# Kernel optimization log

Measured on AMD Instinct MI355X. Metric: run time of the kernel, lower is better.

## Reference

```python
import jax, jax.numpy as jnp
import numpy as np

B, T = 32, 2048
STATE, ACT, LAT, ENC = 128, 16, 256, 1024  # input_dim = STATE + 2*ACT = 160


def setup_inputs() -> dict:
    key = jax.random.key(0)
    ks = jax.random.split(key, 16)
    s = lambda k, shp, sc=0.05: jax.random.normal(k, shp, dtype=jnp.float32) * sc
    return {
        "padded_input": jax.random.normal(ks[0], (B, T, STATE + 2 * ACT), dtype=jnp.float32),
        "enc_w1": s(ks[1], (STATE, ENC)), "enc_b1": s(ks[2], (ENC,)),
        "enc_w2": s(ks[3], (ENC, ENC)),   "enc_b2": s(ks[4], (ENC,)),
        "enc_w3": s(ks[5], (ENC, LAT)),   "enc_b3": s(ks[6], (LAT,)),
        "a_diag": jax.random.uniform(ks[7], (LAT,), minval=-0.8, maxval=0.8, dtype=jnp.float32),
        "B_w": s(ks[8], (ACT, LAT)),
        "dec_w1": s(ks[9], (LAT, ENC)),  "dec_b1": s(ks[10], (ENC,)),
        "dec_w2": s(ks[11], (ENC, ENC)), "dec_b2": s(ks[12], (ENC,)),
        "dec_w3": s(ks[13], (ENC, STATE)), "dec_b3": s(ks[14], (STATE,)),
        "nwarmup": 4,
    }


def reference(padded_input, enc_w1, enc_b1, enc_w2, enc_b2, enc_w3, enc_b3,
              a_diag, B_w, dec_w1, dec_b1, dec_w2, dec_b2, dec_w3, dec_b3,
              nwarmup):
    # slice state / actuator channels
    x_t = padded_input[:, :, :STATE]                      # [B,T,STATE]
    u_t1 = padded_input[:, :, STATE + ACT:]               # [B,T,ACT]

    def encoder(x):
        h = jnp.tanh(x @ enc_w1 + enc_b1)
        h = jnp.tanh(h @ enc_w2 + enc_b2)
        return jnp.tanh(h @ enc_w3 + enc_b3)

    def decoder(z):
        h = jnp.tanh(z @ dec_w1 + dec_b1)
        h = jnp.tanh(h @ dec_w2 + dec_b2)
        return h @ dec_w3 + dec_b3

    z_t = encoder(x_t)                                    # [B,T,LAT]
    a = jnp.clip(a_diag, -0.95, 0.95)                     # clamped diagonal of A
    Bu = u_t1 @ B_w                                       # [B,T,LAT]

    # diagonal linear recurrence with warmup resets (reset_probability=0)
    zT = jnp.swapaxes(z_t, 0, 1)                          # [T,B,LAT]
    BuT = jnp.swapaxes(Bu, 0, 1)                          # [T,B,LAT]
    ts = jnp.arange(T)

    def step(prev, inputs):
        z, bu, t = inputs
        inp = jnp.where(t <= nwarmup, z, prev)
        out = a * inp + bu
        return out, out

    _, outs = jax.lax.scan(step, z_t[:, 0, :], (zT, BuT, ts))
    z_t1 = jnp.swapaxes(outs, 0, 1)                       # [B,T,LAT]
    return decoder(z_t1)                                  # [B,T,STATE]
```

## Files before the change

### kernel.cpp

```cpp
#include <hip/hip_runtime.h>
#include <stdint.h>
#include <type_traits>

#define B_ 32
#define T_ 2048
#define STATE_ 128
#define ACT_ 16
#define LAT_ 256
#define ENC_ 1024
#define ROWS_ (B_ * T_)
#define TENC_ 128
#define MENC_ (B_ * TENC_)
#define NCHUNK_ 64
#define LCHUNK_ 32
#define SLAB_ 32768

using bf16x8 = __attribute__((ext_vector_type(8))) short;
using f32x4  = __attribute__((ext_vector_type(4))) float;
using f32x16 = __attribute__((ext_vector_type(16))) float;

__device__ __forceinline__ uint16_t f2bf(float f) {
  uint32_t u = __float_as_uint(f);
  u += 0x7fff + ((u >> 16) & 1);
  return (uint16_t)(u >> 16);
}

__device__ __forceinline__ float fast_tanh(float x) {
  float e = __expf(2.f * x);
  return 1.f - 2.f / (e + 1.f);
}

__device__ __forceinline__ void xcd_remap(int gx, int gy, int& bm, int& bn) {
  if (((gy & 7) == 0) && ((gx & (gx - 1)) == 0)) {
    const int lin  = blockIdx.y * gx + blockIdx.x;
    const int xcd  = lin & 7;
    const int slot = lin >> 3;
    const int lgx  = 31 - __clz(gx);
    bn = slot & (gx - 1);
    bm = ((slot >> lgx) << 3) + xcd;
  } else {
    bm = blockIdx.y;
    bn = blockIdx.x;
  }
}

template <bool TANH, typename OUT_T>
__device__ __forceinline__ void store4(OUT_T* C, size_t m, int N, int nb,
                                       const float* bias, f32x4 a) {
  const float4 bv = *(const float4*)(bias + nb);
  float v0 = a[0] + bv.x, v1 = a[1] + bv.y, v2 = a[2] + bv.z, v3 = a[3] + bv.w;
  if (TANH) {
    v0 = fast_tanh(v0); v1 = fast_tanh(v1);
    v2 = fast_tanh(v2); v3 = fast_tanh(v3);
  }
  if constexpr (std::is_same<OUT_T, uint16_t>::value) {
    uint32_t p0 = (uint32_t)f2bf(v0) | ((uint32_t)f2bf(v1) << 16);
    uint32_t p1 = (uint32_t)f2bf(v2) | ((uint32_t)f2bf(v3) << 16);
    uint2 p = {p0, p1};
    *(uint2*)(C + m * N + nb) = p;
  } else {
    float4 p = {v0, v1, v2, v3};
    *(float4*)(C + m * N + nb) = p;
  }
}

template <bool TANH, typename OUT_T>
__global__ __launch_bounds__(256) void gemm_bt(
    const uint16_t* __restrict__ A, const uint16_t* __restrict__ Bt,
    const float* __restrict__ bias, OUT_T* __restrict__ C,
    int M, int N, int K) {
  __shared__ uint16_t smA[128 * 64];
  __shared__ uint16_t smB[128 * 64];
  const int tid  = threadIdx.x;
  const int lane = tid & 63;
  const int wave = tid >> 6;
  const int wm = wave >> 1, wn = wave & 1;
  const int l32 = lane & 31, h = lane >> 5;

  int bm, bn;
  xcd_remap(gridDim.x, gridDim.y, bm, bn);
  const int m0 = bm * 128;
  const int n0 = bn * 128;

  const int srow = wave * 32 + (lane >> 3);
  const int sblk = lane & 7;

  f32x16 acc[2][2];
#pragma unroll
  for (int i = 0; i < 2; ++i)
#pragma unroll
    for (int j = 0; j < 2; ++j)
#pragma unroll
      for (int r = 0; r < 16; ++r) acc[i][j][r] = 0.f;

  for (int k0 = 0; k0 < K; k0 += 64) {
#pragma unroll
    for (int i = 0; i < 4; ++i) {
      const int r  = srow + i * 8;
      const int kb = sblk ^ (r & 7);
      const uint16_t* ga = A  + (size_t)(m0 + r) * K + (k0 + kb * 8);
      const uint16_t* gb = Bt + (size_t)(n0 + r) * K + (k0 + kb * 8);
      uint16_t* la = smA + (size_t)(wave * 32 + i * 8) * 64;
      uint16_t* lb = smB + (size_t)(wave * 32 + i * 8) * 64;
      __builtin_amdgcn_global_load_lds(
          (const __attribute__((address_space(1))) void*)ga,
          (__attribute__((address_space(3))) void*)la, 16, 0, 0);
      __builtin_amdgcn_global_load_lds(
          (const __attribute__((address_space(1))) void*)gb,
          (__attribute__((address_space(3))) void*)lb, 16, 0, 0);
    }
    __syncthreads();

#pragma unroll
    for (int ks = 0; ks < 4; ++ks) {
      bf16x8 af[2], bfr[2];
      const int kslot = ks * 2 + h;
#pragma unroll
      for (int mt = 0; mt < 2; ++mt) {
        const int row  = wm * 64 + mt * 32 + l32;
        const int slot = kslot ^ (row & 7);
        af[mt] = *(const bf16x8*)(smA + (size_t)row * 64 + slot * 8);
      }
#pragma unroll
      for (int nt = 0; nt < 2; ++nt) {
        const int row  = wn * 64 + nt * 32 + l32;
        const int slot = kslot ^ (row & 7);
        bfr[nt] = *(const bf16x8*)(smB + (size_t)row * 64 + slot * 8);
      }
#pragma unroll
      for (int mt = 0; mt < 2; ++mt)
#pragma unroll
        for (int nt = 0; nt < 2; ++nt)
          acc[mt][nt] = __builtin_amdgcn_mfma_f32_32x32x16_bf16(
              bfr[nt], af[mt], acc[mt][nt], 0, 0, 0);
    }
    __syncthreads();
  }

#pragma unroll
  for (int mt = 0; mt < 2; ++mt) {
    const size_t m = m0 + wm * 64 + mt * 32 + l32;
#pragma unroll
    for (int nt = 0; nt < 2; ++nt) {
#pragma unroll
      for (int q = 0; q < 4; ++q) {
        const int nb = n0 + wn * 64 + nt * 32 + q * 8 + h * 4;
        f32x4 v = {acc[mt][nt][4 * q + 0], acc[mt][nt][4 * q + 1],
                   acc[mt][nt][4 * q + 2], acc[mt][nt][4 * q + 3]};
        store4<TANH>(C, m, N, nb, bias, v);
      }
    }
  }
}

template <bool TANH, typename OUT_T>
__global__ __launch_bounds__(256, 2) void gemm_wide(
    const uint16_t* __restrict__ A, const uint16_t* __restrict__ Bt,
    const float* __restrict__ bias, OUT_T* __restrict__ C,
    int M, int N, int K) {
  __shared__ uint16_t smA[128 * 64];
  __shared__ uint16_t smB[256 * 64];
  const int tid  = threadIdx.x;
  const int lane = tid & 63;
  const int wave = tid >> 6;
  const int wm = wave >> 1, wn = wave & 1;
  const int l32 = lane & 31, h = lane >> 5;

  int bm, bn;
  xcd_remap(gridDim.x, gridDim.y, bm, bn);
  const int m0 = bm * 128;
  const int n0 = bn * 256;

  const int sr8  = lane >> 3;
  const int sblk = lane & 7;

  f32x16 acc[2][4];
#pragma unroll
  for (int i = 0; i < 2; ++i)
#pragma unroll
    for (int j = 0; j < 4; ++j)
#pragma unroll
      for (int r = 0; r < 16; ++r) acc[i][j][r] = 0.f;

  for (int k0 = 0; k0 < K; k0 += 64) {
#pragma unroll
    for (int i = 0; i < 4; ++i) {
      const int r  = wave * 32 + sr8 + i * 8;
      const int kb = sblk ^ (r & 7);
      const uint16_t* ga = A + (size_t)(m0 + r) * K + (k0 + kb * 8);
      uint16_t* la = smA + (size_t)r * 64;
      __builtin_amdgcn_global_load_lds(
          (const __attribute__((address_space(1))) void*)ga,
          (__attribute__((address_space(3))) void*)la, 16, 0, 0);
    }
#pragma unroll
    for (int i = 0; i < 8; ++i) {
      const int r  = wave * 64 + sr8 + i * 8;
      const int kb = sblk ^ (r & 7);
      const uint16_t* gb = Bt + (size_t)(n0 + r) * K + (k0 + kb * 8);
      uint16_t* lb = smB + (size_t)r * 64;
      __builtin_amdgcn_global_load_lds(
          (const __attribute__((address_space(1))) void*)gb,
          (__attribute__((address_space(3))) void*)lb, 16, 0, 0);
    }
    __syncthreads();

#pragma unroll
    for (int ks = 0; ks < 4; ++ks) {
      bf16x8 af[2], bfr[4];
      const int kslot = ks * 2 + h;
#pragma unroll
      for (int mt = 0; mt < 2; ++mt) {
        const int row  = wm * 64 + mt * 32 + l32;
        const int slot = kslot ^ (row & 7);
        af[mt] = *(const bf16x8*)(smA + (size_t)row * 64 + slot * 8);
      }
#pragma unroll
      for (int nt = 0; nt < 4; ++nt) {
        const int row  = wn * 128 + nt * 32 + l32;
        const int slot = kslot ^ (row & 7);
        bfr[nt] = *(const bf16x8*)(smB + (size_t)row * 64 + slot * 8);
      }
#pragma unroll
      for (int mt = 0; mt < 2; ++mt)
#pragma unroll
        for (int nt = 0; nt < 4; ++nt)
          acc[mt][nt] = __builtin_amdgcn_mfma_f32_32x32x16_bf16(
              bfr[nt], af[mt], acc[mt][nt], 0, 0, 0);
    }
    __syncthreads();
  }

#pragma unroll
  for (int mt = 0; mt < 2; ++mt) {
    const size_t m = m0 + wm * 64 + mt * 32 + l32;
#pragma unroll
    for (int nt = 0; nt < 4; ++nt) {
#pragma unroll
      for (int q = 0; q < 4; ++q) {
        const int nb = n0 + wn * 128 + nt * 32 + q * 8 + h * 4;
        f32x4 v = {acc[mt][nt][4 * q + 0], acc[mt][nt][4 * q + 1],
                   acc[mt][nt][4 * q + 2], acc[mt][nt][4 * q + 3]};
        store4<TANH>(C, m, N, nb, bias, v);
      }
    }
  }
}

template <bool TANH, typename OUT_T>
__global__ __launch_bounds__(256) void gemm64(
    const uint16_t* __restrict__ A, const uint16_t* __restrict__ Bt,
    const float* __restrict__ bias, OUT_T* __restrict__ C,
    int M, int N, int K) {
  __shared__ uint16_t smA[64 * 64];
  __shared__ uint16_t smB[128 * 64];
  const int tid  = threadIdx.x;
  const int lane = tid & 63;
  const int wave = tid >> 6;
  const int wm = wave >> 1, wn = wave & 1;
  const int lr = lane & 15, quad = lane >> 4;

  int bm, bn;
  xcd_remap(gridDim.x, gridDim.y, bm, bn);
  const int m0 = bm * 64;
  const int n0 = bn * 128;

  const int sr8  = lane >> 3;
  const int sblk = lane & 7;

  f32x4 vzero = {0.f, 0.f, 0.f, 0.f};
  f32x4 acc[2][4];
#pragma unroll
  for (int i = 0; i < 2; ++i)
#pragma unroll
    for (int j = 0; j < 4; ++j) acc[i][j] = vzero;

  for (int k0 = 0; k0 < K; k0 += 64) {
#pragma unroll
    for (int i = 0; i < 2; ++i) {
      const int r  = wave * 16 + sr8 + i * 8;
      const int kb = sblk ^ (r & 7);
      const uint16_t* ga = A + (size_t)(m0 + r) * K + (k0 + kb * 8);
      uint16_t* la = smA + (size_t)r * 64;
      __builtin_amdgcn_global_load_lds(
          (const __attribute__((address_space(1))) void*)ga,
          (__attribute__((address_space(3))) void*)la, 16, 0, 0);
    }
#pragma unroll
    for (int i = 0; i < 4; ++i) {
      const int r  = wave * 32 + sr8 + i * 8;
      const int kb = sblk ^ (r & 7);
      const uint16_t* gb = Bt + (size_t)(n0 + r) * K + (k0 + kb * 8);
      uint16_t* lb = smB + (size_t)r * 64;
      __builtin_amdgcn_global_load_lds(
          (const __attribute__((address_space(1))) void*)gb,
          (__attribute__((address_space(3))) void*)lb, 16, 0, 0);
    }
    __syncthreads();

#pragma unroll
    for (int ks = 0; ks < 2; ++ks) {
      bf16x8 af[2], bfr[4];
      const int slotx = (ks * 4 + quad);
#pragma unroll
      for (int mt = 0; mt < 2; ++mt) {
        const int row  = wm * 32 + mt * 16 + lr;
        const int slot = slotx ^ (lr & 7);
        af[mt] = *(const bf16x8*)(smA + (size_t)row * 64 + slot * 8);
      }
#pragma unroll
      for (int nt = 0; nt < 4; ++nt) {
        const int row  = wn * 64 + nt * 16 + lr;
        const int slot = slotx ^ (lr & 7);
        bfr[nt] = *(const bf16x8*)(smB + (size_t)row * 64 + slot * 8);
      }
#pragma unroll
      for (int mt = 0; mt < 2; ++mt)
#pragma unroll
        for (int nt = 0; nt < 4; ++nt)
          acc[mt][nt] = __builtin_amdgcn_mfma_f32_16x16x32_bf16(
              bfr[nt], af[mt], acc[mt][nt], 0, 0, 0);
    }
    __syncthreads();
  }

#pragma unroll
  for (int mt = 0; mt < 2; ++mt) {
    const size_t m = m0 + wm * 32 + mt * 16 + lr;
#pragma unroll
    for (int nt = 0; nt < 4; ++nt) {
      const int nb = n0 + wn * 64 + nt * 16 + quad * 4;
      store4<TANH>(C, m, N, nb, bias, acc[mt][nt]);
    }
  }
}

struct TArgs {
  const float* s[6];
  uint16_t* d[6];
  int R[6];
  int C[6];
};

__global__ __launch_bounds__(256) void transpose_cast(TArgs a) {
  __shared__ float tile[32][33];
  const int z = blockIdx.z;
  const float* s = a.s[z];
  uint16_t* d = a.d[z];
  const int R = a.R[z], C = a.C[z];
  const int bc = blockIdx.x * 32, br = blockIdx.y * 32;
  if (bc >= C || br >= R) return;
  const int tx = threadIdx.x & 31, ty = threadIdx.x >> 5;
#pragma unroll
  for (int i = 0; i < 32; i += 8)
    tile[ty + i][tx] = s[(size_t)(br + ty + i) * C + (bc + tx)];
  __syncthreads();
#pragma unroll
  for (int i = 0; i < 32; i += 8)
    d[(size_t)(bc + ty + i) * R + (br + tx)] = f2bf(tile[tx][ty + i]);
}

__global__ __launch_bounds__(256) void cast_x(const float* __restrict__ pin,
                                              uint16_t* __restrict__ Xc) {
  const int idx = blockIdx.x * 256 + threadIdx.x;
  const int r = idx >> 7, c = idx & 127;
  const int b = r >> 7, t = r & 127;
  Xc[idx] = f2bf(pin[((size_t)b * T_ + t) * 160 + c]);
}

__device__ __forceinline__ float clip_a(const float* a_diag, int l) {
  return fminf(fmaxf(a_diag[l], -0.95f), 0.95f);
}

__device__ __forceinline__ float bu_at(const float* __restrict__ pin, int b,
                                       int t, const float* bw) {
  const float* u = pin + ((size_t)b * T_ + t) * 160 + 144;
  float bu = 0.f;
#pragma unroll
  for (int k = 0; k < ACT_; ++k) bu += u[k] * bw[k];
  return bu;
}

__global__ __launch_bounds__(256) void rec_pass1(
    const float* __restrict__ Zc, const float* __restrict__ pin,
    const float* __restrict__ Bw, const float* __restrict__ a_diag,
    const int* __restrict__ nwp, float* __restrict__ F) {
  const int l = threadIdx.x, c = blockIdx.x, b = blockIdx.y;
  const int nw = *nwp;
  const float a = clip_a(a_diag, l);
  float bw[ACT_];
#pragma unroll
  for (int k = 0; k < ACT_; ++k) bw[k] = Bw[k * LAT_ + l];

  float s = (c == 0) ? Zc[(size_t)b * TENC_ * LAT_ + l] : 0.f;
  const int t0 = c * LCHUNK_;
  for (int j = 0; j < LCHUNK_; ++j) {
    const int t = t0 + j;
    float inp;
    if (t <= nw) {
      const int tt = t < TENC_ ? t : TENC_ - 1;
      inp = Zc[((size_t)b * TENC_ + tt) * LAT_ + l];
    } else {
      inp = s;
    }
    s = a * inp + bu_at(pin, b, t, bw);
  }
  F[((size_t)c * B_ + b) * LAT_ + l] = s;
}

__global__ __launch_bounds__(256) void rec_pass2(
    const float* __restrict__ Zc, const float* __restrict__ F,
    const float* __restrict__ a_diag, const int* __restrict__ nwp,
    float* __restrict__ I) {
  const int l = threadIdx.x, b = blockIdx.x;
  const int nw = *nwp;
  const float a = clip_a(a_diag, l);
  float aL = a;
#pragma unroll
  for (int i = 0; i < 5; ++i) aL *= aL;
  float s = Zc[(size_t)b * TENC_ * LAT_ + l];
  I[(size_t)b * LAT_ + l] = s;
  for (int c = 1; c < NCHUNK_; ++c) {
    const float Fp = F[((size_t)(c - 1) * B_ + b) * LAT_ + l];
    const bool exact = ((c - 1) == 0) || (nw >= (c - 1) * LCHUNK_);
    s = exact ? Fp : (aL * s + Fp);
    I[((size_t)c * B_ + b) * LAT_ + l] = s;
  }
}

__global__ __launch_bounds__(256) void rec_pass3(
    const float* __restrict__ Zc, const float* __restrict__ pin,
    const float* __restrict__ Bw, const float* __restrict__ a_diag,
    const int* __restrict__ nwp, const float* __restrict__ I,
    uint16_t* __restrict__ Zp) {
  const int l = threadIdx.x, c = blockIdx.x, b = blockIdx.y;
  const int nw = *nwp;
  const float a = clip_a(a_diag, l);
  float bw[ACT_];
#pragma unroll
  for (int k = 0; k < ACT_; ++k) bw[k] = Bw[k * LAT_ + l];

  float s = I[((size_t)c * B_ + b) * LAT_ + l];
  const int t0 = c * LCHUNK_;
  for (int j = 0; j < LCHUNK_; ++j) {
    const int t = t0 + j;
    float inp;
    if (t <= nw) {
      const int tt = t < TENC_ ? t : TENC_ - 1;
      inp = Zc[((size_t)b * TENC_ + tt) * LAT_ + l];
    } else {
      inp = s;
    }
    s = a * inp + bu_at(pin, b, t, bw);
    Zp[((size_t)b * T_ + t) * LAT_ + l] = f2bf(s);
  }
}

extern "C" void kernel_launch(void* const* d_in, const int* in_sizes, int n_in,
                              void* d_out, int out_size, void* d_ws,
                              size_t ws_size, hipStream_t stream) {
  const float* pin = (const float*)d_in[0];
  const float* ew1 = (const float*)d_in[1];
  const float* eb1 = (const float*)d_in[2];
  const float* ew2 = (const float*)d_in[3];
  const float* eb2 = (const float*)d_in[4];
  const float* ew3 = (const float*)d_in[5];
  const float* eb3 = (const float*)d_in[6];
  const float* adg = (const float*)d_in[7];
  const float* Bw  = (const float*)d_in[8];
  const float* dw1 = (const float*)d_in[9];
  const float* db1 = (const float*)d_in[10];
  const float* dw2 = (const float*)d_in[11];
  const float* db2 = (const float*)d_in[12];
  const float* dw3 = (const float*)d_in[13];
  const float* db3 = (const float*)d_in[14];
  const int* nwp   = (const int*)d_in[15];
  float* out = (float*)d_out;

  uint8_t* ws = (uint8_t*)d_ws;
  size_t off = 0;
  auto alloc = [&](size_t b) -> void* {
    void* p = ws + off;
    off += (b + 255) & ~(size_t)255;
    return p;
  };
  uint16_t* W1t = (uint16_t*)alloc((size_t)ENC_ * STATE_ * 2);
  uint16_t* W2t = (uint16_t*)alloc((size_t)ENC_ * ENC_ * 2);
  uint16_t* W3t = (uint16_t*)alloc((size_t)LAT_ * ENC_ * 2);
  uint16_t* D1t = (uint16_t*)alloc((size_t)ENC_ * LAT_ * 2);
  uint16_t* D2t = (uint16_t*)alloc((size_t)ENC_ * ENC_ * 2);
  uint16_t* D3t = (uint16_t*)alloc((size_t)STATE_ * ENC_ * 2);
  uint16_t* Xc  = (uint16_t*)alloc((size_t)MENC_ * STATE_ * 2);
  float* Zc = (float*)alloc((size_t)MENC_ * LAT_ * 4);
  float* F  = (float*)alloc((size_t)NCHUNK_ * B_ * LAT_ * 4);
  float* I  = (float*)alloc((size_t)NCHUNK_ * B_ * LAT_ * 4);
  uint16_t* Zp = (uint16_t*)alloc((size_t)ROWS_ * LAT_ * 2);

  const size_t full_g = (size_t)ROWS_ * ENC_ * 2;
  int slab_rows, nslab;
  if (ws_size >= off + 2 * (full_g + 256)) {
    slab_rows = ROWS_;  nslab = 1;
  } else {
    slab_rows = SLAB_;  nslab = 2;
  }
  uint16_t* G1 = (uint16_t*)alloc((size_t)slab_rows * ENC_ * 2);
  uint16_t* G2 = (uint16_t*)alloc((size_t)slab_rows * ENC_ * 2);
  uint16_t* H1c = G1;
  uint16_t* H2c = G1 + (size_t)MENC_ * ENC_;

  if (ws_size < off) return;

  TArgs ta;
  ta.s[0] = ew1; ta.d[0] = W1t; ta.R[0] = STATE_; ta.C[0] = ENC_;
  ta.s[1] = ew2; ta.d[1] = W2t; ta.R[1] = ENC_;   ta.C[1] = ENC_;
  ta.s[2] = ew3; ta.d[2] = W3t; ta.R[2] = ENC_;   ta.C[2] = LAT_;
  ta.s[3] = dw1; ta.d[3] = D1t; ta.R[3] = LAT_;   ta.C[3] = ENC_;
  ta.s[4] = dw2; ta.d[4] = D2t; ta.R[4] = ENC_;   ta.C[4] = ENC_;
  ta.s[5] = dw3; ta.d[5] = D3t; ta.R[5] = ENC_;   ta.C[5] = STATE_;
  transpose_cast<<<dim3(32, 32, 6), 256, 0, stream>>>(ta);

  cast_x<<<dim3((MENC_ * STATE_) / 256), 256, 0, stream>>>(pin, Xc);

  gemm_bt<true, uint16_t><<<dim3(ENC_ / 128, MENC_ / 128), 256, 0, stream>>>(
      Xc, W1t, eb1, H1c, MENC_, ENC_, STATE_);
  gemm_bt<true, uint16_t><<<dim3(ENC_ / 128, MENC_ / 128), 256, 0, stream>>>(
      H1c, W2t, eb2, H2c, MENC_, ENC_, ENC_);
  gemm64<true, float><<<dim3(LAT_ / 128, MENC_ / 64), 256, 0, stream>>>(
      H2c, W3t, eb3, Zc, MENC_, LAT_, ENC_);

  rec_pass1<<<dim3(NCHUNK_, B_), 256, 0, stream>>>(Zc, pin, Bw, adg, nwp, F);
  rec_pass2<<<dim3(B_), 256, 0, stream>>>(Zc, F, adg, nwp, I);
  rec_pass3<<<dim3(NCHUNK_, B_), 256, 0, stream>>>(Zc, pin, Bw, adg, nwp, I,
                                                   Zp);

  for (int s = 0; s < nslab; ++s) {
    const uint16_t* Zs = Zp + (size_t)s * slab_rows * LAT_;
    float* Os = out + (size_t)s * slab_rows * STATE_;
    gemm_wide<true, uint16_t><<<dim3(ENC_ / 256, slab_rows / 128), 256, 0,
                                stream>>>(Zs, D1t, db1, G1, slab_rows, ENC_,
                                          LAT_);
    gemm_wide<true, uint16_t><<<dim3(ENC_ / 256, slab_rows / 128), 256, 0,
                                stream>>>(G1, D2t, db2, G2, slab_rows, ENC_,
                                          ENC_);
    gemm64<false, float><<<dim3(STATE_ / 128, slab_rows / 64), 256, 0,
                           stream>>>(G2, D3t, db3, Os, slab_rows, STATE_,
                                     ENC_);
  }
}
```

Before: 508.4 us.

## Replace decoder wide GEMM with 256x256 double-buffered 8-wave pipelined kernel

Replaces the 128x256-tile, single-buffered decoder GEMM with a 256x256-tile kernel that uses 512 threads (8 waves), double-buffered LDS, and a hand-scheduled ping-pong of LDS loads, global-to-LDS prefetches and 16x16x32 MFMA bursts with raw barriers and setprio. The goal is to hide global load latency behind MFMA work and raise arithmetic intensity per tile for the two large decoder layers. The cost is 128 KB of LDS per block and intricate manual vmcnt/barrier accounting that can break if the tile math is off, plus fewer blocks in the grid.

```diff
diff --git a/kernel.cpp b/kernel.cpp
--- a/kernel.cpp
+++ b/kernel.cpp
@@ -154,95 +154,149 @@
 }
 
 template <bool TANH, typename OUT_T>
-__global__ __launch_bounds__(256, 2) void gemm_wide(
+__global__ __launch_bounds__(512, 2) void gemm256(
     const uint16_t* __restrict__ A, const uint16_t* __restrict__ Bt,
     const float* __restrict__ bias, OUT_T* __restrict__ C,
     int M, int N, int K) {
-  __shared__ uint16_t smA[128 * 64];
-  __shared__ uint16_t smB[256 * 64];
+  __shared__ uint16_t smA[2 * 2 * 128 * 64];
+  __shared__ uint16_t smB[2 * 2 * 128 * 64];
   const int tid  = threadIdx.x;
-  const int lane = tid & 63;
-  const int wave = tid >> 6;
-  const int wm = wave >> 1, wn = wave & 1;
-  const int l32 = lane & 31, h = lane >> 5;
+  const int l    = tid & 63;
+  const int wv   = tid >> 6;
+  const int wm   = wv >> 2;
+  const int wn   = wv & 3;
+  const int lr   = l & 15, quad = l >> 4;
+  const int x7   = lr & 7;
 
   int bm, bn;
   xcd_remap(gridDim.x, gridDim.y, bm, bn);
-  const int m0 = bm * 128;
+  const int m0 = bm * 256;
   const int n0 = bn * 256;
 
-  const int sr8  = lane >> 3;
-  const int sblk = lane & 7;
-
-  f32x16 acc[2][4];
-#pragma unroll
-  for (int i = 0; i < 2; ++i)
-#pragma unroll
-    for (int j = 0; j < 4; ++j)
-#pragma unroll
-      for (int r = 0; r < 16; ++r) acc[i][j][r] = 0.f;
-
-  for (int k0 = 0; k0 < K; k0 += 64) {
-#pragma unroll
-    for (int i = 0; i < 4; ++i) {
-      const int r  = wave * 32 + sr8 + i * 8;
-      const int kb = sblk ^ (r & 7);
-      const uint16_t* ga = A + (size_t)(m0 + r) * K + (k0 + kb * 8);
-      uint16_t* la = smA + (size_t)r * 64;
+  const int jr0 = wv * 16 + (l >> 3);
+  const int kbe = ((l & 7) ^ (l >> 3)) * 8;
+  int garow[2], gbrow[2];
+#pragma unroll
+  for (int i = 0; i < 2; ++i) {
+    const int jr = jr0 + i * 8;
+    garow[i] = (jr & 63) + ((jr >> 6) * 128);
+    gbrow[i] = (jr & 31) + ((jr >> 5) * 64);
+  }
+  const int NT = K >> 6;
+
+  const int arow = wm * 64 + lr;
+  const int brow = wn * 32 + lr;
+
+  f32x4 acc[8][4];
+#pragma unroll
+  for (int i = 0; i < 8; ++i)
+#pragma unroll
+    for (int j = 0; j < 4; ++j) acc[i][j] = f32x4{0.f, 0.f, 0.f, 0.f};
+
+  bf16x8 af[4][2];
+  bf16x8 bf0[2][2];
+  bf16x8 bf1[2][2];
+
+  auto stA = [&](int t, int h, int par) {
+#pragma unroll
+    for (int i = 0; i < 2; ++i) {
+      const uint16_t* g =
+          A + (size_t)(m0 + garow[i] + h * 64) * K + (t * 64 + kbe);
+      uint16_t* d = smA + (size_t)((par * 2 + h) * 128 + wv * 16 + i * 8) * 64;
       __builtin_amdgcn_global_load_lds(
-          (const __attribute__((address_space(1))) void*)ga,
-          (__attribute__((address_space(3))) void*)la, 16, 0, 0);
-    }
-#pragma unroll
-    for (int i = 0; i < 8; ++i) {
-      const int r  = wave * 64 + sr8 + i * 8;
-      const int kb = sblk ^ (r & 7);
-      const uint16_t* gb = Bt + (size_t)(n0 + r) * K + (k0 + kb * 8);
-      uint16_t* lb = smB + (size_t)r * 64;
+          (const __attribute__((address_space(1))) void*)g,
+          (__attribute__((address_space(3))) void*)d, 16, 0, 0);
+    }
+  };
+  auto stB = [&](int t, int h, int par) {
+#pragma unroll
+    for (int i = 0; i < 2; ++i) {
+      const uint16_t* g =
+          Bt + (size_t)(n0 + gbrow[i] + h * 32) * K + (t * 64 + kbe);
+      uint16_t* d = smB + (size_t)((par * 2 + h) * 128 + wv * 16 + i * 8) * 64;
       __builtin_amdgcn_global_load_lds(
-          (const __attribute__((address_space(1))) void*)gb,
-          (__attribute__((address_space(3))) void*)lb, 16, 0, 0);
-    }
-    __syncthreads();
-
-#pragma unroll
-    for (int ks = 0; ks < 4; ++ks) {
-      bf16x8 af[2], bfr[4];
-      const int kslot = ks * 2 + h;
-#pragma unroll
-      for (int mt = 0; mt < 2; ++mt) {
-        const int row  = wm * 64 + mt * 32 + l32;
-        const int slot = kslot ^ (row & 7);
-        af[mt] = *(const bf16x8*)(smA + (size_t)row * 64 + slot * 8);
-      }
-#pragma unroll
-      for (int nt = 0; nt < 4; ++nt) {
-        const int row  = wn * 128 + nt * 32 + l32;
-        const int slot = kslot ^ (row & 7);
-        bfr[nt] = *(const bf16x8*)(smB + (size_t)row * 64 + slot * 8);
-      }
-#pragma unroll
-      for (int mt = 0; mt < 2; ++mt)
-#pragma unroll
-        for (int nt = 0; nt < 4; ++nt)
-          acc[mt][nt] = __builtin_amdgcn_mfma_f32_32x32x16_bf16(
-              bfr[nt], af[mt], acc[mt][nt], 0, 0, 0);
-    }
-    __syncthreads();
-  }
-
-#pragma unroll
-  for (int mt = 0; mt < 2; ++mt) {
-    const size_t m = m0 + wm * 64 + mt * 32 + l32;
-#pragma unroll
-    for (int nt = 0; nt < 4; ++nt) {
-#pragma unroll
-      for (int q = 0; q < 4; ++q) {
-        const int nb = n0 + wn * 128 + nt * 32 + q * 8 + h * 4;
-        f32x4 v = {acc[mt][nt][4 * q + 0], acc[mt][nt][4 * q + 1],
-                   acc[mt][nt][4 * q + 2], acc[mt][nt][4 * q + 3]};
-        store4<TANH>(C, m, N, nb, bias, v);
-      }
+          (const __attribute__((address_space(1))) void*)g,
+          (__attribute__((address_space(3))) void*)d, 16, 0, 0);
+    }
+  };
+  auto ldA = [&](int rh, int par) {
+#pragma unroll
+    for (int f = 0; f < 4; ++f)
+#pragma unroll
+      for (int ks = 0; ks < 2; ++ks)
+        af[f][ks] = *(const bf16x8*)(smA +
+            (size_t)((par * 2 + rh) * 128 + arow + f * 16) * 64 +
+            ((ks * 4 + quad) ^ x7) * 8);
+  };
+  auto ldB = [&](int ch, int par, bf16x8 (&dst)[2][2]) {
+#pragma unroll
+    for (int c2 = 0; c2 < 2; ++c2)
+#pragma unroll
+      for (int ks = 0; ks < 2; ++ks)
+        dst[c2][ks] = *(const bf16x8*)(smB +
+            (size_t)((par * 2 + ch) * 128 + brow + c2 * 16) * 64 +
+            ((ks * 4 + quad) ^ x7) * 8);
+  };
+  auto mm = [&](int rh, int ch, bf16x8 (&bfr)[2][2]) {
+#pragma unroll
+    for (int ks = 0; ks < 2; ++ks)
+#pragma unroll
+      for (int f = 0; f < 4; ++f)
+#pragma unroll
+        for (int c2 = 0; c2 < 2; ++c2)
+          acc[rh * 4 + f][ch * 2 + c2] =
+              __builtin_amdgcn_mfma_f32_16x16x32_bf16(
+                  bfr[c2][ks], af[f][ks], acc[rh * 4 + f][ch * 2 + c2],
+                  0, 0, 0);
+  };
+
+#define BARRIER() asm volatile("s_barrier" ::: "memory")
+#define WLGKM0()  asm volatile("s_waitcnt lgkmcnt(0)" ::: "memory")
+
+  stA(0, 0, 0); stB(0, 0, 0); stB(0, 1, 0); stA(0, 1, 0);
+  if (NT > 1) { stA(1, 0, 1); stB(1, 0, 1); stB(1, 1, 1); }
+  asm volatile("s_waitcnt vmcnt(6)" ::: "memory");
+  BARRIER();
+
+  auto window = [&](int w, int par) {
+    ldA(0, par);
+    ldB(0, par, bf0);
+    if (w + 1 < NT) stA(w + 1, 1, par ^ 1);
+    BARRIER(); WLGKM0();
+    __builtin_amdgcn_s_setprio(1); mm(0, 0, bf0); __builtin_amdgcn_s_setprio(0);
+    BARRIER();
+    ldB(1, par, bf1);
+    if (w + 2 < NT) stA(w + 2, 0, par);
+    BARRIER(); WLGKM0();
+    __builtin_amdgcn_s_setprio(1); mm(0, 1, bf1); __builtin_amdgcn_s_setprio(0);
+    BARRIER();
+    ldA(1, par);
+    if (w + 2 < NT) stB(w + 2, 0, par);
+    BARRIER(); WLGKM0();
+    __builtin_amdgcn_s_setprio(1); mm(1, 1, bf1); __builtin_amdgcn_s_setprio(0);
+    BARRIER();
+    if (w + 2 < NT) stB(w + 2, 1, par);
+    __builtin_amdgcn_s_setprio(1); mm(1, 0, bf0); __builtin_amdgcn_s_setprio(0);
+    if (w + 2 < NT) asm volatile("s_waitcnt vmcnt(6)" ::: "memory");
+    else            asm volatile("s_waitcnt vmcnt(0)" ::: "memory");
+    BARRIER();
+  };
+
+  for (int w = 0; w < NT; w += 2) {
+    window(w, 0);
+    window(w + 1, 1);
+  }
+
+#undef BARRIER
+#undef WLGKM0
+
+#pragma unroll
+  for (int rf = 0; rf < 8; ++rf) {
+    const size_t m = m0 + wm * 128 + rf * 16 + lr;
+#pragma unroll
+    for (int cf = 0; cf < 4; ++cf) {
+      const int nb = n0 + wn * 64 + cf * 16 + quad * 4;
+      store4<TANH>(C, m, N, nb, bias, acc[rf][cf]);
     }
   }
 }
@@ -536,12 +590,12 @@
   for (int s = 0; s < nslab; ++s) {
     const uint16_t* Zs = Zp + (size_t)s * slab_rows * LAT_;
     float* Os = out + (size_t)s * slab_rows * STATE_;
-    gemm_wide<true, uint16_t><<<dim3(ENC_ / 256, slab_rows / 128), 256, 0,
-                                stream>>>(Zs, D1t, db1, G1, slab_rows, ENC_,
-                                          LAT_);
-    gemm_wide<true, uint16_t><<<dim3(ENC_ / 256, slab_rows / 128), 256, 0,
-                                stream>>>(G1, D2t, db2, G2, slab_rows, ENC_,
-                                          ENC_);
+    gemm256<true, uint16_t><<<dim3(ENC_ / 256, slab_rows / 256), 512, 0,
+                              stream>>>(Zs, D1t, db1, G1, slab_rows, ENC_,
+                                        LAT_);
+    gemm256<true, uint16_t><<<dim3(ENC_ / 256, slab_rows / 256), 512, 0,
+                              stream>>>(G1, D2t, db2, G2, slab_rows, ENC_,
+                                        ENC_);
     gemm64<false, float><<<dim3(STATE_ / 128, slab_rows / 64), 256, 0,
                            stream>>>(G2, D3t, db3, Os, slab_rows, STATE_,
                                      ENC_);
```

Measured after the change: 504.2 us. No clear change (-0.8%).

## Add 256x256 ping-pong pipelined GEMM for decoder second layer

Applied to the files above, without the earlier changes.

Adds a new 512-thread GEMM kernel with 256x256 output tiles, double-buffered LDS filled by direct global-to-LDS loads, XOR-swizzled LDS reads, and a windowed schedule that interleaves half-tile loads with MFMA bursts under raised wave priority. The decoder's 1024x1024 layer switches to it. The aim is more data reuse per tile and better overlap of memory traffic with matrix math on the largest GEMM. In exchange it uses larger LDS and register footprints, and the hand-tuned waitcnt/barrier schedule is fragile.

```diff
diff --git a/kernel.cpp b/kernel.cpp
--- a/kernel.cpp
+++ b/kernel.cpp
@@ -241,6 +241,155 @@
         const int nb = n0 + wn * 128 + nt * 32 + q * 8 + h * 4;
         f32x4 v = {acc[mt][nt][4 * q + 0], acc[mt][nt][4 * q + 1],
                    acc[mt][nt][4 * q + 2], acc[mt][nt][4 * q + 3]};
+        store4<TANH>(C, m, N, nb, bias, v);
+      }
+    }
+  }
+}
+
+template <bool TANH, typename OUT_T>
+__global__ __launch_bounds__(512, 2) void gemm256(
+    const uint16_t* __restrict__ A, const uint16_t* __restrict__ Bt,
+    const float* __restrict__ bias, OUT_T* __restrict__ C,
+    int M, int N, int K) {
+  __shared__ uint16_t smA[2 * 2 * 128 * 64];
+  __shared__ uint16_t smB[2 * 2 * 128 * 64];
+  const int tid  = threadIdx.x;
+  const int l    = tid & 63;
+  const int wv   = tid >> 6;
+  const int wm   = wv >> 2;
+  const int wn   = wv & 3;
+  const int l32  = l & 31, h = l >> 5;
+  const int x7   = l32 & 7;
+
+  int bm, bn;
+  xcd_remap(gridDim.x, gridDim.y, bm, bn);
+  const int m0 = bm * 256;
+  const int n0 = bn * 256;
+
+  const int jr0 = wv * 16 + (l >> 3);
+  const int kbe = ((l & 7) ^ (l >> 3)) * 8;
+  int garow[2], gbrow[2];
+#pragma unroll
+  for (int i = 0; i < 2; ++i) {
+    const int jr = jr0 + i * 8;
+    garow[i] = (jr & 63) + ((jr >> 6) * 128);
+    gbrow[i] = (jr & 31) + ((jr >> 5) * 64);
+  }
+  const int NT = K >> 6;
+
+  const int arow = wm * 64 + l32;
+  const int brow = wn * 32 + l32;
+
+  f32x16 acc[4][2];
+#pragma unroll
+  for (int i = 0; i < 4; ++i)
+#pragma unroll
+    for (int j = 0; j < 2; ++j)
+#pragma unroll
+      for (int r = 0; r < 16; ++r) acc[i][j][r] = 0.f;
+
+  bf16x8 af[2][4];
+  bf16x8 bf0[4];
+  bf16x8 bf1[4];
+
+  auto stA = [&](int t, int hh, int par) {
+#pragma unroll
+    for (int i = 0; i < 2; ++i) {
+      const uint16_t* g =
+          A + (size_t)(m0 + garow[i] + hh * 64) * K + (t * 64 + kbe);
+      uint16_t* d = smA + (size_t)((par * 2 + hh) * 128 + wv * 16 + i * 8) * 64;
+      __builtin_amdgcn_global_load_lds(
+          (const __attribute__((address_space(1))) void*)g,
+          (__attribute__((address_space(3))) void*)d, 16, 0, 0);
+    }
+  };
+  auto stB = [&](int t, int hh, int par) {
+#pragma unroll
+    for (int i = 0; i < 2; ++i) {
+      const uint16_t* g =
+          Bt + (size_t)(n0 + gbrow[i] + hh * 32) * K + (t * 64 + kbe);
+      uint16_t* d = smB + (size_t)((par * 2 + hh) * 128 + wv * 16 + i * 8) * 64;
+      __builtin_amdgcn_global_load_lds(
+          (const __attribute__((address_space(1))) void*)g,
+          (__attribute__((address_space(3))) void*)d, 16, 0, 0);
+    }
+  };
+  auto ldA = [&](int rh, int par) {
+#pragma unroll
+    for (int fa = 0; fa < 2; ++fa)
+#pragma unroll
+      for (int ks = 0; ks < 4; ++ks)
+        af[fa][ks] = *(const bf16x8*)(smA +
+            (size_t)((par * 2 + rh) * 128 + arow + fa * 32) * 64 +
+            (((ks * 2 + h) ^ x7) * 8));
+  };
+  auto ldB = [&](int ch, int par, bf16x8 (&dst)[4]) {
+#pragma unroll
+    for (int ks = 0; ks < 4; ++ks)
+      dst[ks] = *(const bf16x8*)(smB +
+          (size_t)((par * 2 + ch) * 128 + brow) * 64 +
+          (((ks * 2 + h) ^ x7) * 8));
+  };
+  auto mm = [&](int rh, int ch, bf16x8 (&bfr)[4]) {
+#pragma unroll
+    for (int ks = 0; ks < 4; ++ks)
+#pragma unroll
+      for (int fa = 0; fa < 2; ++fa)
+        acc[rh * 2 + fa][ch] = __builtin_amdgcn_mfma_f32_32x32x16_bf16(
+            bfr[ks], af[fa][ks], acc[rh * 2 + fa][ch], 0, 0, 0);
+  };
+
+#define BARRIER() asm volatile("s_barrier" ::: "memory")
+#define WLGKM0()  asm volatile("s_waitcnt lgkmcnt(0)" ::: "memory")
+
+  stA(0, 0, 0); stB(0, 0, 0); stB(0, 1, 0); stA(0, 1, 0);
+  if (NT > 1) { stA(1, 0, 1); stB(1, 0, 1); stB(1, 1, 1); }
+  asm volatile("s_waitcnt vmcnt(6)" ::: "memory");
+  BARRIER();
+
+  auto window = [&](int w, int par) {
+    ldA(0, par);
+    ldB(0, par, bf0);
+    if (w + 1 < NT) stA(w + 1, 1, par ^ 1);
+    BARRIER(); WLGKM0();
+    __builtin_amdgcn_s_setprio(1); mm(0, 0, bf0); __builtin_amdgcn_s_setprio(0);
+    BARRIER();
+    ldB(1, par, bf1);
+    if (w + 2 < NT) stA(w + 2, 0, par);
+    BARRIER(); WLGKM0();
+    __builtin_amdgcn_s_setprio(1); mm(0, 1, bf1); __builtin_amdgcn_s_setprio(0);
+    BARRIER();
+    ldA(1, par);
+    if (w + 2 < NT) stB(w + 2, 0, par);
+    BARRIER(); WLGKM0();
+    __builtin_amdgcn_s_setprio(1); mm(1, 1, bf1); __builtin_amdgcn_s_setprio(0);
+    BARRIER();
+    if (w + 2 < NT) stB(w + 2, 1, par);
+    __builtin_amdgcn_s_setprio(1); mm(1, 0, bf0); __builtin_amdgcn_s_setprio(0);
+    if (w + 2 < NT) asm volatile("s_waitcnt vmcnt(6)" ::: "memory");
+    else            asm volatile("s_waitcnt vmcnt(0)" ::: "memory");
+    BARRIER();
+  };
+
+  for (int w = 0; w < NT; w += 2) {
+    window(w, 0);
+    window(w + 1, 1);
+  }
+
+#undef BARRIER
+#undef WLGKM0
+
+#pragma unroll
+  for (int amf = 0; amf < 4; ++amf) {
+    const size_t m = m0 + wm * 128 + (amf >> 1) * 64 + (amf & 1) * 32 + l32;
+#pragma unroll
+    for (int ch = 0; ch < 2; ++ch) {
+#pragma unroll
+      for (int q = 0; q < 4; ++q) {
+        const int nb = n0 + wn * 64 + ch * 32 + q * 8 + h * 4;
+        f32x4 v = {acc[amf][ch][4 * q + 0], acc[amf][ch][4 * q + 1],
+                   acc[amf][ch][4 * q + 2], acc[amf][ch][4 * q + 3]};
         store4<TANH>(C, m, N, nb, bias, v);
       }
     }
@@ -539,9 +688,9 @@
     gemm_wide<true, uint16_t><<<dim3(ENC_ / 256, slab_rows / 128), 256, 0,
                                 stream>>>(Zs, D1t, db1, G1, slab_rows, ENC_,
                                           LAT_);
-    gemm_wide<true, uint16_t><<<dim3(ENC_ / 256, slab_rows / 128), 256, 0,
-                                stream>>>(G1, D2t, db2, G2, slab_rows, ENC_,
-                                          ENC_);
+    gemm256<true, uint16_t><<<dim3(ENC_ / 256, slab_rows / 256), 512, 0,
+                              stream>>>(G1, D2t, db2, G2, slab_rows, ENC_,
+                                        ENC_);
     gemm64<false, float><<<dim3(STATE_ / 128, slab_rows / 64), 256, 0,
                            stream>>>(G2, D3t, db3, Os, slab_rows, STATE_,
                                      ENC_);
```

New measurement: 523.8 us. 1.03x slower.
